# Performance work log

Hardware: AMD Instinct MI355X
Metric: run time of the kernel (lower is better)

The kernel has to match this reference:

```python
import jax, jax.numpy as jnp
import numpy as np

TOKENS, D_IN, D_OUT, R = 8192, 4096, 4096, 16
SCALE = 2.0

def setup_inputs() -> dict:
    key = jax.random.key(0)
    ks = jax.random.split(key, 5)
    return {
        "x": jax.random.normal(ks[0], (TOKENS, D_IN), dtype=jnp.float32),
        "weight": jax.random.normal(ks[1], (D_OUT, D_IN), dtype=jnp.float32) * 0.02,
        "bias": jax.random.normal(ks[2], (D_OUT,), dtype=jnp.float32) * 0.01,
        "lora_A": jax.random.normal(ks[3], (R, D_IN), dtype=jnp.float32) * 0.02,
        "lora_B": jax.random.normal(ks[4], (D_OUT, R), dtype=jnp.float32) * 0.02,
    }

def reference(x, weight, bias, lora_A, lora_B):
    # y = x W^T + bias + scale * x (B A)^T
    # Reassociate to avoid materializing the [D_OUT, D_IN] B@A matrix:
    # x (B A)^T = (x A^T) B^T  -- same math, low-rank path.
    base = jnp.einsum('ti,oi->to', x, weight) + bias          # [T, D_OUT]
    lora = jnp.einsum('tr,or->to', jnp.einsum('ti,ri->tr', x, lora_A), lora_B)
    return base + SCALE * lora
```

## Files before the change

kernel.cpp:

```cpp
#include <hip/hip_runtime.h>
#include <hip/hip_bf16.h>
#include <stdint.h>

#define TOKENS 8192
#define DIN 4096
#define DOUT 4096
#define RNK 16
#define LORA_SCALE 2.0f

typedef __attribute__((ext_vector_type(8))) __bf16 bf16x8;
typedef __attribute__((ext_vector_type(4))) float f32x4;

__device__ __forceinline__ unsigned short f2bf(float f) {
    union { float f; unsigned int u; } v; v.f = f;
    unsigned int u = v.u;
    unsigned int r = (u + 0x7fffu + ((u >> 16) & 1u)) >> 16;
    return (unsigned short)r;
}

__device__ __forceinline__ void async_copy16(const void* g, void* l) {
    __builtin_amdgcn_global_load_lds(
        (const __attribute__((address_space(1))) void*)g,
        (__attribute__((address_space(3))) void*)l,
        16, 0, 0);
}

__global__ void cast_x_kernel(const float4* __restrict__ x, ushort4* __restrict__ xb) {
    int i = blockIdx.x * blockDim.x + threadIdx.x;
    float4 v = x[i];
    ushort4 o;
    o.x = f2bf(v.x); o.y = f2bf(v.y); o.z = f2bf(v.z); o.w = f2bf(v.w);
    xb[i] = o;
}

__global__ void fold_w_kernel(const float* __restrict__ W,
                              const float* __restrict__ lA,
                              const float* __restrict__ lB,
                              ushort* __restrict__ Wb) {
    int o  = blockIdx.y;
    int i0 = (blockIdx.x * blockDim.x + threadIdx.x) * 4;
    __shared__ float sB[RNK];
    if (threadIdx.x < RNK) sB[threadIdx.x] = lB[(size_t)o * RNK + threadIdx.x];
    __syncthreads();
    float4 w = *(const float4*)(W + (size_t)o * DIN + i0);
    float ax = 0.f, ay = 0.f, az = 0.f, aw = 0.f;
#pragma unroll
    for (int r = 0; r < RNK; r++) {
        float4 a = *(const float4*)(lA + (size_t)r * DIN + i0);
        float b = sB[r];
        ax += b * a.x; ay += b * a.y; az += b * a.z; aw += b * a.w;
    }
    ushort4 outv;
    outv.x = f2bf(w.x + LORA_SCALE * ax);
    outv.y = f2bf(w.y + LORA_SCALE * ay);
    outv.z = f2bf(w.z + LORA_SCALE * az);
    outv.w = f2bf(w.w + LORA_SCALE * aw);
    *(ushort4*)(Wb + (size_t)o * DIN + i0) = outv;
}

#define BM 256
#define BN 256
#define BK 32
#define NTILES (DIN / BK)
#define SLOT_U16 16384
#define SLOT_BYTES 32768
#define B_OFF_BYTES 16384

__global__ __launch_bounds__(512, 2) void gemm_bias_kernel(
    const ushort* __restrict__ Xb, const ushort* __restrict__ Wb,
    const float* __restrict__ bias, float* __restrict__ Y) {

    __shared__ ushort smem[4 * SLOT_U16];

    const int tid  = threadIdx.x;
    const int lane = tid & 63;
    const int wave = tid >> 6;

    const int bid  = blockIdx.x;
    const int sbid = (bid & 7) * 64 + (bid >> 3);
    const int m0 = (sbid >> 4) * BM;
    const int n0 = (sbid & 15) * BN;

    const int wm = (wave >> 2) * 128;
    const int wn = (wave & 3) * 64;

    auto srcoff = [](int ci) -> size_t {
        const int L = ci >> 3, p = ci & 7;
        const int u = p ^ (L & 7);
        return (size_t)(2 * L + (u >> 2)) * DIN + (size_t)((u & 3) * 8);
    };
    const ushort* pA0 = Xb + (size_t)m0 * DIN + srcoff(tid);
    const ushort* pA1 = Xb + (size_t)m0 * DIN + srcoff(tid + 512);
    const ushort* pB0 = Wb + (size_t)n0 * DIN + srcoff(tid);
    const ushort* pB1 = Wb + (size_t)n0 * DIN + srcoff(tid + 512);

#define STAGE_A(slot) do { \
        ushort* d_ = smem + (slot) * SLOT_U16 + tid * 8; \
        async_copy16(pA0, d_); async_copy16(pA1, d_ + 4096); \
        pA0 += BK; pA1 += BK; } while (0)
#define STAGE_B(slot) do { \
        ushort* d_ = smem + (slot) * SLOT_U16 + 8192 + tid * 8; \
        async_copy16(pB0, d_); async_copy16(pB1, d_ + 4096); \
        pB0 += BK; pB1 += BK; } while (0)

    const int lr = lane & 15, qq = lane >> 4;
    const int pp = (qq + 4 * (lr & 1)) ^ ((lr >> 1) & 7);
    const int offA = ((wm >> 1) + (lr >> 1)) * 128 + pp * 16;
    const int offB = ((wn >> 1) + (lr >> 1)) * 128 + pp * 16;
    const char* smemc = (const char*)smem;

    f32x4 acc[8][4] = {};
    bf16x8 af[4], bfr[4];

    STAGE_A(0); STAGE_B(0);
    STAGE_A(1); STAGE_B(1);
    STAGE_A(2); STAGE_B(2);
    asm volatile("s_waitcnt vmcnt(8)" ::: "memory");
    __builtin_amdgcn_s_barrier();

#pragma unroll 1
    for (int t = 0; t < NTILES; ++t) {
        const char* sa = smemc + (size_t)(t & 3) * SLOT_BYTES;
        const char* sb = sa + B_OFF_BYTES;
        const int  stslot  = (t + 3) & 3;
        const bool doStage = (t + 3 < NTILES);

#pragma unroll
        for (int f = 0; f < 4; f++) af[f]  = *(const bf16x8*)(sa + offA + f * 1024);
#pragma unroll
        for (int f = 0; f < 4; f++) bfr[f] = *(const bf16x8*)(sb + offB + f * 1024);
        if (doStage) STAGE_A(stslot);
        __builtin_amdgcn_s_barrier();
        asm volatile("s_waitcnt lgkmcnt(0)" ::: "memory");
        __builtin_amdgcn_s_setprio(1);
#pragma unroll
        for (int mf = 0; mf < 4; mf++)
#pragma unroll
            for (int nf = 0; nf < 4; nf++)
                acc[mf][nf] = __builtin_amdgcn_mfma_f32_16x16x32_bf16(
                    af[mf], bfr[nf], acc[mf][nf], 0, 0, 0);
        __builtin_amdgcn_s_setprio(0);
        __builtin_amdgcn_s_barrier();

#pragma unroll
        for (int f = 0; f < 4; f++) af[f] = *(const bf16x8*)(sa + offA + (4 + f) * 1024);
        if (doStage) STAGE_B(stslot);
        __builtin_amdgcn_s_barrier();
        asm volatile("s_waitcnt lgkmcnt(0)" ::: "memory");
        __builtin_amdgcn_s_setprio(1);
#pragma unroll
        for (int mf = 0; mf < 4; mf++)
#pragma unroll
            for (int nf = 0; nf < 4; nf++)
                acc[4 + mf][nf] = __builtin_amdgcn_mfma_f32_16x16x32_bf16(
                    af[mf], bfr[nf], acc[4 + mf][nf], 0, 0, 0);
        __builtin_amdgcn_s_setprio(0);

        if (t + 3 < NTILES) {
            asm volatile("s_waitcnt vmcnt(8)" ::: "memory");
            __builtin_amdgcn_s_barrier();
        } else if (t + 3 == NTILES) {
            asm volatile("s_waitcnt vmcnt(4)" ::: "memory");
            __builtin_amdgcn_s_barrier();
        } else if (t + 2 == NTILES) {
            asm volatile("s_waitcnt vmcnt(0)" ::: "memory");
            __builtin_amdgcn_s_barrier();
        }
    }

    const int col  = lane & 15;
    const int qrow = (lane >> 4) * 4;
#pragma unroll
    for (int nf = 0; nf < 4; nf++) {
        const int n = n0 + wn + nf * 16 + col;
        const float bv = bias[n];
#pragma unroll
        for (int mf = 0; mf < 8; mf++) {
            const int m = m0 + wm + mf * 16 + qrow;
            float* yp = Y + (size_t)m * DOUT + n;
            yp[0]                  = acc[mf][nf].x + bv;
            yp[(size_t)DOUT]       = acc[mf][nf].y + bv;
            yp[2 * (size_t)DOUT]   = acc[mf][nf].z + bv;
            yp[3 * (size_t)DOUT]   = acc[mf][nf].w + bv;
        }
    }
#undef STAGE_A
#undef STAGE_B
}

extern "C" void kernel_launch(void* const* d_in, const int* in_sizes, int n_in,
                              void* d_out, int out_size, void* d_ws, size_t ws_size,
                              hipStream_t stream) {
    const float* x    = (const float*)d_in[0];
    const float* W    = (const float*)d_in[1];
    const float* bias = (const float*)d_in[2];
    const float* lA   = (const float*)d_in[3];
    const float* lB   = (const float*)d_in[4];
    float* Y = (float*)d_out;

    ushort* xb = (ushort*)d_ws;
    ushort* wb = xb + (size_t)TOKENS * DIN;

    cast_x_kernel<<<(TOKENS * DIN / 4) / 256, 256, 0, stream>>>(
        (const float4*)x, (ushort4*)xb);
    fold_w_kernel<<<dim3(DIN / (256 * 4), DOUT), 256, 0, stream>>>(W, lA, lB, wb);
    gemm_bias_kernel<<<dim3((TOKENS / BM) * (DOUT / BN)), 512, 0, stream>>>(
        xb, wb, bias, Y);
}
```

Measured before the change: 550.1 us.

## Prefetch next tile's LDS fragments into registers, drop intra-iteration barriers, fuse prep kernels

The GEMM main loop now double-buffers its register fragments. The second A half goes into a separate register set, and the next tile's A and B fragments are loaded from LDS while the current tile's MFMAs run. This lets the two mid-iteration barriers and the lgkmcnt waits be removed. The vmcnt thresholds are changed so the next tile is already resident when it is read. The cast and fold prep kernels are merged into a single launch to save one kernel launch, at the cost of higher register pressure in the GEMM.

```diff
diff --git a/kernel.cpp b/kernel.cpp
--- a/kernel.cpp
+++ b/kernel.cpp
@@ -25,37 +25,43 @@
         16, 0, 0);
 }
 
-__global__ void cast_x_kernel(const float4* __restrict__ x, ushort4* __restrict__ xb) {
-    int i = blockIdx.x * blockDim.x + threadIdx.x;
-    float4 v = x[i];
-    ushort4 o;
-    o.x = f2bf(v.x); o.y = f2bf(v.y); o.z = f2bf(v.z); o.w = f2bf(v.w);
-    xb[i] = o;
-}
-
-__global__ void fold_w_kernel(const float* __restrict__ W,
-                              const float* __restrict__ lA,
-                              const float* __restrict__ lB,
-                              ushort* __restrict__ Wb) {
-    int o  = blockIdx.y;
-    int i0 = (blockIdx.x * blockDim.x + threadIdx.x) * 4;
+#define CAST_BLOCKS (TOKENS * DIN / 4 / 256)
+#define FOLD_BLOCKS ((DIN / (256 * 4)) * DOUT)
+
+__global__ void prep_kernel(const float4* __restrict__ x, ushort4* __restrict__ xb,
+                            const float* __restrict__ W,
+                            const float* __restrict__ lA,
+                            const float* __restrict__ lB,
+                            ushort* __restrict__ Wb) {
     __shared__ float sB[RNK];
-    if (threadIdx.x < RNK) sB[threadIdx.x] = lB[(size_t)o * RNK + threadIdx.x];
-    __syncthreads();
-    float4 w = *(const float4*)(W + (size_t)o * DIN + i0);
-    float ax = 0.f, ay = 0.f, az = 0.f, aw = 0.f;
-#pragma unroll
-    for (int r = 0; r < RNK; r++) {
-        float4 a = *(const float4*)(lA + (size_t)r * DIN + i0);
-        float b = sB[r];
-        ax += b * a.x; ay += b * a.y; az += b * a.z; aw += b * a.w;
+    const int b = blockIdx.x;
+    if (b < CAST_BLOCKS) {
+        int i = b * 256 + threadIdx.x;
+        float4 v = x[i];
+        ushort4 o;
+        o.x = f2bf(v.x); o.y = f2bf(v.y); o.z = f2bf(v.z); o.w = f2bf(v.w);
+        xb[i] = o;
+    } else {
+        const int bb = b - CAST_BLOCKS;
+        const int o  = bb >> 2;
+        const int i0 = ((bb & 3) * 256 + threadIdx.x) * 4;
+        if (threadIdx.x < RNK) sB[threadIdx.x] = lB[(size_t)o * RNK + threadIdx.x];
+        __syncthreads();
+        float4 w = *(const float4*)(W + (size_t)o * DIN + i0);
+        float ax = 0.f, ay = 0.f, az = 0.f, aw = 0.f;
+#pragma unroll
+        for (int r = 0; r < RNK; r++) {
+            float4 a = *(const float4*)(lA + (size_t)r * DIN + i0);
+            float bv = sB[r];
+            ax += bv * a.x; ay += bv * a.y; az += bv * a.z; aw += bv * a.w;
+        }
+        ushort4 outv;
+        outv.x = f2bf(w.x + LORA_SCALE * ax);
+        outv.y = f2bf(w.y + LORA_SCALE * ay);
+        outv.z = f2bf(w.z + LORA_SCALE * az);
+        outv.w = f2bf(w.w + LORA_SCALE * aw);
+        *(ushort4*)(Wb + (size_t)o * DIN + i0) = outv;
     }
-    ushort4 outv;
-    outv.x = f2bf(w.x + LORA_SCALE * ax);
-    outv.y = f2bf(w.y + LORA_SCALE * ay);
-    outv.z = f2bf(w.z + LORA_SCALE * az);
-    outv.w = f2bf(w.w + LORA_SCALE * aw);
-    *(ushort4*)(Wb + (size_t)o * DIN + i0) = outv;
 }
 
 #define BM 256
@@ -106,32 +112,35 @@
     const int lr = lane & 15, qq = lane >> 4;
     const int pp = (qq + 4 * (lr & 1)) ^ ((lr >> 1) & 7);
     const int offA = ((wm >> 1) + (lr >> 1)) * 128 + pp * 16;
-    const int offB = ((wn >> 1) + (lr >> 1)) * 128 + pp * 16;
+    const int offB = B_OFF_BYTES + ((wn >> 1) + (lr >> 1)) * 128 + pp * 16;
     const char* smemc = (const char*)smem;
 
     f32x4 acc[8][4] = {};
-    bf16x8 af[4], bfr[4];
+    bf16x8 af[4], af2[4], bfr[4];
 
     STAGE_A(0); STAGE_B(0);
     STAGE_A(1); STAGE_B(1);
     STAGE_A(2); STAGE_B(2);
-    asm volatile("s_waitcnt vmcnt(8)" ::: "memory");
+    asm volatile("s_waitcnt vmcnt(4)" ::: "memory");
     __builtin_amdgcn_s_barrier();
+
+#pragma unroll
+    for (int f = 0; f < 4; f++) af[f]  = *(const bf16x8*)(smemc + offA + f * 1024);
+#pragma unroll
+    for (int f = 0; f < 4; f++) bfr[f] = *(const bf16x8*)(smemc + offB + f * 1024);
 
 #pragma unroll 1
     for (int t = 0; t < NTILES; ++t) {
-        const char* sa = smemc + (size_t)(t & 3) * SLOT_BYTES;
-        const char* sb = sa + B_OFF_BYTES;
+        const char* sa  = smemc + (size_t)(t & 3) * SLOT_BYTES;
+        const char* saN = smemc + (size_t)((t + 1) & 3) * SLOT_BYTES;
         const int  stslot  = (t + 3) & 3;
         const bool doStage = (t + 3 < NTILES);
-
-#pragma unroll
-        for (int f = 0; f < 4; f++) af[f]  = *(const bf16x8*)(sa + offA + f * 1024);
-#pragma unroll
-        for (int f = 0; f < 4; f++) bfr[f] = *(const bf16x8*)(sb + offB + f * 1024);
+        const bool haveNext = (t + 1 < NTILES);
+
+#pragma unroll
+        for (int f = 0; f < 4; f++)
+            af2[f] = *(const bf16x8*)(sa + offA + (4 + f) * 1024);
         if (doStage) STAGE_A(stslot);
-        __builtin_amdgcn_s_barrier();
-        asm volatile("s_waitcnt lgkmcnt(0)" ::: "memory");
         __builtin_amdgcn_s_setprio(1);
 #pragma unroll
         for (int mf = 0; mf < 4; mf++)
@@ -140,29 +149,32 @@
                 acc[mf][nf] = __builtin_amdgcn_mfma_f32_16x16x32_bf16(
                     af[mf], bfr[nf], acc[mf][nf], 0, 0, 0);
         __builtin_amdgcn_s_setprio(0);
-        __builtin_amdgcn_s_barrier();
-
-#pragma unroll
-        for (int f = 0; f < 4; f++) af[f] = *(const bf16x8*)(sa + offA + (4 + f) * 1024);
+
+        if (haveNext) {
+#pragma unroll
+            for (int f = 0; f < 4; f++)
+                af[f] = *(const bf16x8*)(saN + offA + f * 1024);
+        }
         if (doStage) STAGE_B(stslot);
-        __builtin_amdgcn_s_barrier();
-        asm volatile("s_waitcnt lgkmcnt(0)" ::: "memory");
         __builtin_amdgcn_s_setprio(1);
 #pragma unroll
         for (int mf = 0; mf < 4; mf++)
 #pragma unroll
             for (int nf = 0; nf < 4; nf++)
                 acc[4 + mf][nf] = __builtin_amdgcn_mfma_f32_16x16x32_bf16(
-                    af[mf], bfr[nf], acc[4 + mf][nf], 0, 0, 0);
+                    af2[mf], bfr[nf], acc[4 + mf][nf], 0, 0, 0);
         __builtin_amdgcn_s_setprio(0);
 
-        if (t + 3 < NTILES) {
-            asm volatile("s_waitcnt vmcnt(8)" ::: "memory");
-            __builtin_amdgcn_s_barrier();
-        } else if (t + 3 == NTILES) {
+        if (haveNext) {
+#pragma unroll
+            for (int f = 0; f < 4; f++)
+                bfr[f] = *(const bf16x8*)(saN + offB + f * 1024);
+        }
+
+        if (t < NTILES - 3) {
             asm volatile("s_waitcnt vmcnt(4)" ::: "memory");
             __builtin_amdgcn_s_barrier();
-        } else if (t + 2 == NTILES) {
+        } else if (t == NTILES - 3) {
             asm volatile("s_waitcnt vmcnt(0)" ::: "memory");
             __builtin_amdgcn_s_barrier();
         }
@@ -201,9 +213,8 @@
     ushort* xb = (ushort*)d_ws;
     ushort* wb = xb + (size_t)TOKENS * DIN;
 
-    cast_x_kernel<<<(TOKENS * DIN / 4) / 256, 256, 0, stream>>>(
-        (const float4*)x, (ushort4*)xb);
-    fold_w_kernel<<<dim3(DIN / (256 * 4), DOUT), 256, 0, stream>>>(W, lA, lB, wb);
+    prep_kernel<<<CAST_BLOCKS + FOLD_BLOCKS, 256, 0, stream>>>(
+        (const float4*)x, (ushort4*)xb, W, lA, lB, wb);
     gemm_bias_kernel<<<dim3((TOKENS / BM) * (DOUT / BN)), 512, 0, stream>>>(
         xb, wb, bias, Y);
 }
```

Measured after the change: 551.5 us. About the same (+0.3%).
